# Kernel tuning notes

Hardware: AMD Instinct MI355X
Metric: run time of the kernel (lower is better)

The kernel has to match this reference:

```python
import jax, jax.numpy as jnp
import numpy as np

BS, P, D, D_WM, H, W = 64, 512, 1024, 1024, 16, 128
HD = D_WM // H
SCALE = 1.0 / np.sqrt(HD)


def setup_inputs() -> dict:
    key = jax.random.key(0)
    ks = jax.random.split(key, 10)
    s = 0.02
    x_all = jax.random.normal(ks[0], (BS, P, D), dtype=jnp.float32)
    reset_mask_all = jax.random.randint(ks[1], (BS, P), 0, 50) == 0
    return {
        'x_all': x_all,
        'reset_mask_all': reset_mask_all,
        'Wq_w': jax.random.normal(ks[2], (D, D_WM), dtype=jnp.float32) * s,
        'Wq_b': jnp.zeros((D_WM,), jnp.float32),
        'Wk_w': jax.random.normal(ks[3], (D, D_WM), dtype=jnp.float32) * s,
        'Wk_b': jnp.zeros((D_WM,), jnp.float32),
        'Wv_w': jax.random.normal(ks[4], (D, D_WM), dtype=jnp.float32) * s,
        'Wv_b': jnp.zeros((D_WM,), jnp.float32),
        'Wo_w': jax.random.normal(ks[5], (D_WM, D), dtype=jnp.float32) * s,
        'Wo_b': jnp.zeros((D,), jnp.float32),
    }


def _forward_span(x_all, reset_mask_all, Wq_w, Wq_b, Wk_w, Wk_b, Wv_w, Wv_b, Wo_w, Wo_b):
    # Batched projections over all P tokens (matches forward_span)
    q_all = jnp.einsum('bpd,de->bpe', x_all, Wq_w) + Wq_b
    k_all = jnp.einsum('bpd,de->bpe', x_all, Wk_w) + Wk_b
    v_all = jnp.einsum('bpd,de->bpe', x_all, Wv_w) + Wv_b

    def step(carry, inp):
        K, V, valid, ptr = carry  # [BS,W,D_WM], [BS,W,D_WM], [BS,W] bool, [BS] int
        q, k, v, reset_t = inp    # [BS,D_WM] x3, [BS] bool
        # doc-boundary reset
        valid = valid & ~reset_t[:, None]
        ptr = jnp.where(reset_t, 0, ptr)
        # ring-buffer write at ptr (one-hot broadcast, as in the original)
        wm = jnp.arange(W)[None, :] == ptr[:, None]          # [BS,W] bool
        wf = wm.astype(K.dtype)[:, :, None]                   # [BS,W,1]
        K = K * (1.0 - wf) + k[:, None, :] * wf
        V = V * (1.0 - wf) + v[:, None, :] * wf
        valid = valid | wm
        # windowed multi-head attention over the buffer
        qh = q.reshape(BS, H, HD)
        Kh = K.reshape(BS, W, H, HD)
        Vh = V.reshape(BS, W, H, HD)
        attn = jnp.einsum('bhd,bwhd->bhw', qh, Kh) * SCALE
        attn = jnp.where(valid[:, None, :], attn, -jnp.inf)
        attn = jax.nn.softmax(attn, axis=-1)
        attn = jnp.nan_to_num(attn)
        out = jnp.einsum('bhw,bwhd->bhd', attn, Vh).reshape(BS, D_WM)
        y = out @ Wo_w + Wo_b
        ptr = (ptr + 1) % W
        return (K, V, valid, ptr), y

    init = (
        jnp.zeros((BS, W, D_WM), x_all.dtype),
        jnp.zeros((BS, W, D_WM), x_all.dtype),
        jnp.zeros((BS, W), bool),
        jnp.zeros((BS,), jnp.int32),
    )
    xs = (
        q_all.transpose(1, 0, 2),
        k_all.transpose(1, 0, 2),
        v_all.transpose(1, 0, 2),
        reset_mask_all.T,
    )
    _, ys = jax.lax.scan(step, init, xs)  # ys: [P,BS,D]
    return ys.transpose(1, 0, 2)


def reference(x_all, reset_mask_all, Wq_w, Wq_b, Wk_w, Wk_b, Wv_w, Wv_b, Wo_w, Wo_b):
    return _forward_span(x_all, reset_mask_all, Wq_w, Wq_b, Wk_w, Wk_b, Wv_w, Wv_b, Wo_w, Wo_b)
```

## Files before the change

kernel.cpp:

```cpp
#include <hip/hip_runtime.h>
#include <stdint.h>

typedef __bf16 bf16_t;
typedef __bf16 bf16x8 __attribute__((ext_vector_type(8)));
typedef __bf16 bf16x4 __attribute__((ext_vector_type(4)));
typedef float  f32x4  __attribute__((ext_vector_type(4)));

constexpr int cBS = 64, cP = 512, cD = 1024, cDWM = 1024, cH = 16, cHD = 64, cW = 128;
constexpr int cVTP = 672;
constexpr int cM = cBS * cP;
constexpr float cSCALE = 0.125f;

__device__ __forceinline__ void gld_lds16(const void* g, void* l) {
#if __has_builtin(__builtin_amdgcn_global_load_lds)
  __builtin_amdgcn_global_load_lds(
      (__attribute__((address_space(1))) void*)g,
      (__attribute__((address_space(3))) void*)l, 16, 0, 0);
#else
  *(bf16x8*)l = *(const bf16x8*)g;
#endif
}

__global__ void cvt_x_k(const float* __restrict__ X, bf16_t* __restrict__ Y, int n) {
  int i = (blockIdx.x * blockDim.x + threadIdx.x) * 4;
  if (i >= n) return;
  float4 v = *(const float4*)(X + i);
  bf16x4 o;
  o[0] = (bf16_t)v.x; o[1] = (bf16_t)v.y; o[2] = (bf16_t)v.z; o[3] = (bf16_t)v.w;
  *(bf16x4*)(Y + i) = o;
}

__global__ void cvt_wt_k(const float* __restrict__ W0, const float* __restrict__ W1,
                         const float* __restrict__ W2, const float* __restrict__ W3,
                         bf16_t* __restrict__ T0, bf16_t* __restrict__ T1,
                         bf16_t* __restrict__ T2, bf16_t* __restrict__ T3) {
  __shared__ float tile[32][33];
  const float* Wsrc; bf16_t* Tdst;
  switch (blockIdx.z) {
    case 0: Wsrc = W0; Tdst = T0; break;
    case 1: Wsrc = W1; Tdst = T1; break;
    case 2: Wsrc = W2; Tdst = T2; break;
    default: Wsrc = W3; Tdst = T3; break;
  }
  const int n0 = blockIdx.x * 32, k0 = blockIdx.y * 32;
  const int c = threadIdx.x & 31, r8 = threadIdx.x >> 5;
#pragma unroll
  for (int q = 0; q < 4; ++q) {
    int row = r8 + q * 8;
    tile[row][c] = Wsrc[(size_t)(k0 + row) * 1024 + n0 + c];
  }
  __syncthreads();
#pragma unroll
  for (int q = 0; q < 4; ++q) {
    int row = r8 + q * 8;
    Tdst[(size_t)(n0 + row) * 1024 + k0 + c] = (bf16_t)tile[c][row];
  }
}

__global__ void resets2_k(const int* __restrict__ mask, int* __restrict__ r) {
  __shared__ int sm[cP];
  const int b = blockIdx.x, t = threadIdx.x;
  sm[t] = mask[b * cP + t] ? t : 0;
  __syncthreads();
#pragma unroll
  for (int d = 1; d < cP; d <<= 1) {
    int u = (t >= d) ? sm[t - d] : 0;
    __syncthreads();
    if (u > sm[t]) sm[t] = u;
    __syncthreads();
  }
  r[b * cP + t] = sm[t];
}

__global__ __launch_bounds__(512, 2)
void gemm_qkv8_k(const bf16_t* __restrict__ A, const bf16_t* __restrict__ Wt,
                 const float* __restrict__ bq, const float* __restrict__ bk,
                 const float* __restrict__ bvv,
                 bf16_t* __restrict__ Qh, bf16_t* __restrict__ Kh,
                 bf16_t* __restrict__ Vt) {
  __shared__ __align__(16) char LDS[131072];
  const int tid = threadIdx.x;
  const int wid = tid >> 6, ln = tid & 63;
  const int ln15 = ln & 15, g4 = ln >> 4;
  const int wr = wid >> 2, wc = wid & 3;

  const int g = blockIdx.x + 12 * blockIdx.y;
  const int xcd = g & 7, s = g >> 3;
  const int nb = s % 12, mloc = s / 12;
  const int m0 = (xcd * 16 + mloc) * 256, n0 = nb * 256;

  const bf16_t* Ab = A + (size_t)m0 * 1024;
  const bf16_t* Bb = Wt + (size_t)n0 * 1024;

  const int srow = tid >> 2;
  const int gslot = (tid & 3) ^ (srow & 3);
  const size_t aoff = (size_t)srow * 1024 + (size_t)(gslot * 8);
  char* const lbase = LDS + tid * 16;

  const int slotr = (g4 ^ (ln15 & 3)) << 4;
  const int abase = (wr * 128 + ln15) * 64 + slotr;
  const int bbase = 32768 + (wc * 64 + ln15) * 64 + slotr;

  f32x4 acc[8][4];
#pragma unroll
  for (int i = 0; i < 8; ++i)
#pragma unroll
    for (int j = 0; j < 4; ++j) acc[i][j] = {0.f, 0.f, 0.f, 0.f};

#define STAGE_A(buf, kh, j) do {                                              \
    const bf16_t* gp_ = Ab + (size_t)((j) * 64 + (kh) * 32) + aoff;           \
    char* lp_ = lbase + (buf) * 65536 + (kh) * 16384;                         \
    gld_lds16(gp_, lp_);                                                      \
    gld_lds16(gp_ + (size_t)128 * 1024, lp_ + 8192);                          \
  } while (0)

#define STAGE_B(buf, kh, j) do {                                              \
    const bf16_t* gp_ = Bb + (size_t)((j) * 64 + (kh) * 32) + aoff;           \
    char* lp_ = lbase + (buf) * 65536 + (kh) * 16384 + 32768;                 \
    gld_lds16(gp_, lp_);                                                      \
    gld_lds16(gp_ + (size_t)128 * 1024, lp_ + 8192);                          \
  } while (0)

#define NOSTAGE ((void)0)
#define VM4 asm volatile("s_waitcnt vmcnt(4)" ::: "memory")
#define VM0 asm volatile("s_waitcnt vmcnt(0)" ::: "memory")
#define NOVM ((void)0)

#define PHASE(buf, kh, qm, STAGE, VME) do {                                   \
    const char* Ar_ = LDS + (buf) * 65536 + (kh) * 16384 + abase + (qm) * 4096;\
    const char* Br_ = LDS + (buf) * 65536 + (kh) * 16384 + bbase;             \
    bf16x8 af_[4], bf_[4];                                                    \
    af_[0] = *(const bf16x8*)(Ar_);                                           \
    af_[1] = *(const bf16x8*)(Ar_ + 1024);                                    \
    af_[2] = *(const bf16x8*)(Ar_ + 2048);                                    \
    af_[3] = *(const bf16x8*)(Ar_ + 3072);                                    \
    bf_[0] = *(const bf16x8*)(Br_);                                           \
    bf_[1] = *(const bf16x8*)(Br_ + 1024);                                    \
    bf_[2] = *(const bf16x8*)(Br_ + 2048);                                    \
    bf_[3] = *(const bf16x8*)(Br_ + 3072);                                    \
    STAGE;                                                                    \
    __builtin_amdgcn_s_barrier();                                             \
    asm volatile("s_waitcnt lgkmcnt(0)" ::: "memory");                        \
    __builtin_amdgcn_s_setprio(1);                                            \
    _Pragma("unroll")                                                         \
    for (int mi4_ = 0; mi4_ < 4; ++mi4_)                                      \
      _Pragma("unroll")                                                       \
      for (int nj_ = 0; nj_ < 4; ++nj_)                                       \
        acc[(qm) * 4 + mi4_][nj_] = __builtin_amdgcn_mfma_f32_16x16x32_bf16(  \
            af_[mi4_], bf_[nj_], acc[(qm) * 4 + mi4_][nj_], 0, 0, 0);         \
    __builtin_amdgcn_s_setprio(0);                                            \
    VME;                                                                      \
    __builtin_amdgcn_s_barrier();                                             \
  } while (0)

  STAGE_A(0, 0, 0); STAGE_B(0, 0, 0); STAGE_A(0, 1, 0); STAGE_B(0, 1, 0);
  asm volatile("s_waitcnt vmcnt(4)" ::: "memory");
  __builtin_amdgcn_s_barrier();

  for (int t = 0; t < 7; ++t) {
    const int j1 = 2 * t + 1, j2 = 2 * t + 2;
    PHASE(0, 0, 0, STAGE_A(1, 0, j1), NOVM);
    PHASE(0, 0, 1, STAGE_B(1, 0, j1), VM4);
    PHASE(0, 1, 0, STAGE_A(1, 1, j1), NOVM);
    PHASE(0, 1, 1, STAGE_B(1, 1, j1), VM4);
    PHASE(1, 0, 0, STAGE_A(0, 0, j2), NOVM);
    PHASE(1, 0, 1, STAGE_B(0, 0, j2), VM4);
    PHASE(1, 1, 0, STAGE_A(0, 1, j2), NOVM);
    PHASE(1, 1, 1, STAGE_B(0, 1, j2), VM4);
  }
  PHASE(0, 0, 0, STAGE_A(1, 0, 15), NOVM);
  PHASE(0, 0, 1, STAGE_B(1, 0, 15), VM4);
  PHASE(0, 1, 0, STAGE_A(1, 1, 15), NOVM);
  PHASE(0, 1, 1, STAGE_B(1, 1, 15), VM4);
  PHASE(1, 0, 0, NOSTAGE, NOVM);
  PHASE(1, 0, 1, NOSTAGE, VM0);
  PHASE(1, 1, 0, NOSTAGE, NOVM);
  PHASE(1, 1, 1, NOSTAGE, NOVM);

#undef PHASE
#undef STAGE_A
#undef STAGE_B

  const int seg = n0 >> 10;
  const float* bias = (seg == 0) ? bq : (seg == 1) ? bk : bvv;
  bf16_t* QK = (seg == 0) ? Qh : Kh;
#pragma unroll
  for (int mi = 0; mi < 8; ++mi) {
    const int rbase = m0 + wr * 128 + mi * 16 + g4 * 4;
    const int b = rbase >> 9, pb = rbase & 511;
#pragma unroll
    for (int nj = 0; nj < 4; ++nj) {
      const int col = n0 + wc * 64 + nj * 16 + ln15;
      const int cl = col & 1023;
      const int h = cl >> 6, hd = cl & 63;
      const float bv = bias[cl];
      if (seg < 2) {
#pragma unroll
        for (int r = 0; r < 4; ++r)
          QK[(((size_t)(b * cH + h)) * cP + pb + r) * cHD + hd] =
              (bf16_t)(acc[mi][nj][r] + bv);
      } else {
        bf16x4 pk;
#pragma unroll
        for (int r = 0; r < 4; ++r) pk[r] = (bf16_t)(acc[mi][nj][r] + bv);
        *(bf16x4*)(Vt + ((size_t)((b * cH + h) * cHD + hd)) * cVTP + 128 + pb) = pk;
      }
    }
  }
}

__global__ __launch_bounds__(256)
void gemm_bt_k(const bf16_t* __restrict__ A, const bf16_t* __restrict__ Bt,
               const float* __restrict__ bias, float* __restrict__ C,
               int M, int N, int K) {
  __shared__ __align__(16) bf16_t As[2][128 * 32];
  __shared__ __align__(16) bf16_t Bs[2][128 * 32];
  const int tid = threadIdx.x;
  const int wv = tid >> 6, ln = tid & 63;
  const int ln15 = ln & 15, g4 = ln >> 4;

  const int g = blockIdx.x + 8 * blockIdx.y;
  const int xcd = g & 7, s = g >> 3;
  const int nb = s & 7, mloc = s >> 3;
  const int m0 = (xcd * 32 + mloc) * 128, n0 = nb * 128;

  const int wm = (wv >> 1) * 64, wn = (wv & 1) * 64;
  const bf16_t* Ab = A + (size_t)m0 * K;
  const bf16_t* Bb = Bt + (size_t)n0 * K;

  auto stage = [&](const bf16_t* G, bf16_t* L, int k0) {
#pragma unroll
    for (int gg = 0; gg < 2; ++gg) {
      int slot = gg * 256 + tid;
      gld_lds16(G + (size_t)(slot >> 2) * K + (k0 + (slot & 3) * 8), L + slot * 8);
    }
  };

  f32x4 acc[4][4];
#pragma unroll
  for (int i = 0; i < 4; ++i)
#pragma unroll
    for (int j = 0; j < 4; ++j) acc[i][j] = {0.f, 0.f, 0.f, 0.f};

  const int nk = K >> 5;
  stage(Ab, As[0], 0);
  stage(Bb, Bs[0], 0);
  for (int kt = 0; kt < nk; ++kt) {
    __syncthreads();
    if (kt + 1 < nk) {
      stage(Ab, As[(kt + 1) & 1], (kt + 1) * 32);
      stage(Bb, Bs[(kt + 1) & 1], (kt + 1) * 32);
    }
    const bf16_t* Asb = As[kt & 1];
    const bf16_t* Bsb = Bs[kt & 1];
    bf16x8 af[4], bfr[4];
#pragma unroll
    for (int i = 0; i < 4; ++i)
      af[i] = *(const bf16x8*)(Asb + (wm + i * 16 + ln15) * 32 + g4 * 8);
#pragma unroll
    for (int j = 0; j < 4; ++j)
      bfr[j] = *(const bf16x8*)(Bsb + (wn + j * 16 + ln15) * 32 + g4 * 8);
#pragma unroll
    for (int i = 0; i < 4; ++i)
#pragma unroll
      for (int j = 0; j < 4; ++j)
        acc[i][j] = __builtin_amdgcn_mfma_f32_16x16x32_bf16(af[i], bfr[j], acc[i][j], 0, 0, 0);
  }

#pragma unroll
  for (int i = 0; i < 4; ++i) {
    const int rbase = m0 + wm + i * 16 + g4 * 4;
#pragma unroll
    for (int j = 0; j < 4; ++j) {
      const int col = n0 + wn + j * 16 + ln15;
      const float bv = bias[col];
#pragma unroll
      for (int r = 0; r < 4; ++r)
        C[(size_t)(rbase + r) * N + col] = acc[i][j][r] + bv;
    }
  }
}

__global__ __launch_bounds__(256)
void attn3_k(const bf16_t* __restrict__ Q, const bf16_t* __restrict__ Kv,
             const bf16_t* __restrict__ Vt, const int* __restrict__ rr,
             bf16_t* __restrict__ O) {
  __shared__ __align__(16) bf16_t Pl[4][16][168];
  const int tid = threadIdx.x;
  const int wv = tid >> 6, ln = tid & 63, ln15 = ln & 15, g4 = ln >> 4;
  const int h = blockIdx.x, b = blockIdx.y, tc = blockIdx.z;
  bf16_t(*Pw)[168] = Pl[wv];
  const bf16_t* vb = Vt + ((size_t)(b * cH + h)) * cHD * cVTP;
  const bf16_t* qb = Q + ((size_t)(b * cH + h)) * cP * cHD;
  const bf16_t* kb = Kv + ((size_t)(b * cH + h)) * cP * cHD;

  for (int sub = 0; sub < 2; ++sub) {
    const int t0 = (tc * 2 + sub) * 64 + wv * 16;
    const int sbase = t0 - 128;

    int rv[4];
#pragma unroll
    for (int r = 0; r < 4; ++r) rv[r] = rr[b * cP + t0 + g4 * 4 + r];

    const bf16_t* qp = qb + (size_t)(t0 + ln15) * cHD + g4 * 8;
    const bf16x8 qa0 = *(const bf16x8*)qp;
    const bf16x8 qa1 = *(const bf16x8*)(qp + 32);

    f32x4 lg[9];
#pragma unroll
    for (int c = 0; c < 9; ++c) {
      const int s = sbase + c * 16 + ln15;
      bf16x8 k0v, k1v;
      if ((unsigned)s < (unsigned)cP) {
        const bf16_t* kp = kb + (size_t)s * cHD + g4 * 8;
        k0v = *(const bf16x8*)kp;
        k1v = *(const bf16x8*)(kp + 32);
      } else {
#pragma unroll
        for (int z = 0; z < 8; ++z) { k0v[z] = (bf16_t)0.f; k1v[z] = (bf16_t)0.f; }
      }
      f32x4 a = {0.f, 0.f, 0.f, 0.f};
      a = __builtin_amdgcn_mfma_f32_16x16x32_bf16(qa0, k0v, a, 0, 0, 0);
      a = __builtin_amdgcn_mfma_f32_16x16x32_bf16(qa1, k1v, a, 0, 0, 0);
      lg[c] = a;
    }

    float mx[4] = {-1e30f, -1e30f, -1e30f, -1e30f};
#pragma unroll
    for (int c = 0; c < 9; ++c)
#pragma unroll
      for (int r = 0; r < 4; ++r) {
        const int s = sbase + c * 16 + ln15;
        const int t = t0 + g4 * 4 + r;
        const bool ok = (s >= rv[r]) && (s <= t) && (t - s < cW);
        const float l = ok ? lg[c][r] * cSCALE : -1e30f;
        lg[c][r] = l;
        mx[r] = fmaxf(mx[r], l);
      }
#pragma unroll
    for (int r = 0; r < 4; ++r) {
      mx[r] = fmaxf(mx[r], __shfl_xor(mx[r], 1));
      mx[r] = fmaxf(mx[r], __shfl_xor(mx[r], 2));
      mx[r] = fmaxf(mx[r], __shfl_xor(mx[r], 4));
      mx[r] = fmaxf(mx[r], __shfl_xor(mx[r], 8));
    }
    float sm[4] = {0.f, 0.f, 0.f, 0.f};
#pragma unroll
    for (int c = 0; c < 9; ++c)
#pragma unroll
      for (int r = 0; r < 4; ++r) {
        const float e = __expf(lg[c][r] - mx[r]);
        lg[c][r] = e;
        sm[r] += e;
      }
#pragma unroll
    for (int r = 0; r < 4; ++r) {
      sm[r] += __shfl_xor(sm[r], 1);
      sm[r] += __shfl_xor(sm[r], 2);
      sm[r] += __shfl_xor(sm[r], 4);
      sm[r] += __shfl_xor(sm[r], 8);
    }
    float inv[4];
#pragma unroll
    for (int r = 0; r < 4; ++r) inv[r] = 1.f / sm[r];

#pragma unroll
    for (int c = 0; c < 9; ++c)
#pragma unroll
      for (int r = 0; r < 4; ++r)
        Pw[g4 * 4 + r][c * 16 + ln15] = (bf16_t)(lg[c][r] * inv[r]);
#pragma unroll
    for (int z = 0; z < 4; ++z)
      Pw[ln15][144 + g4 * 4 + z] = (bf16_t)0.f;

    f32x4 oacc[4];
#pragma unroll
    for (int j = 0; j < 4; ++j) oacc[j] = {0.f, 0.f, 0.f, 0.f};
#pragma unroll
    for (int c2 = 0; c2 < 5; ++c2) {
      const bf16x8 pa = *(const bf16x8*)(&Pw[ln15][c2 * 32 + g4 * 8]);
#pragma unroll
      for (int j = 0; j < 4; ++j) {
        const bf16x8 vf =
            *(const bf16x8*)(vb + (size_t)(j * 16 + ln15) * cVTP + (t0 + c2 * 32 + g4 * 8));
        oacc[j] = __builtin_amdgcn_mfma_f32_16x16x32_bf16(pa, vf, oacc[j], 0, 0, 0);
      }
    }
#pragma unroll
    for (int j = 0; j < 4; ++j) {
      const int col = h * cHD + j * 16 + ln15;
#pragma unroll
      for (int r = 0; r < 4; ++r)
        O[((size_t)(b * cP + t0 + g4 * 4 + r)) * cDWM + col] = (bf16_t)oacc[j][r];
    }
  }
}

extern "C" void kernel_launch(void* const* d_in, const int* in_sizes, int n_in,
                              void* d_out, int out_size, void* d_ws, size_t ws_size,
                              hipStream_t stream) {
  (void)in_sizes; (void)n_in; (void)out_size; (void)ws_size;
  const float* x  = (const float*)d_in[0];
  const int* mask = (const int*)d_in[1];
  const float* Wq = (const float*)d_in[2];
  const float* bq = (const float*)d_in[3];
  const float* Wk = (const float*)d_in[4];
  const float* bk = (const float*)d_in[5];
  const float* Wv = (const float*)d_in[6];
  const float* bv = (const float*)d_in[7];
  const float* Wo = (const float*)d_in[8];
  const float* bo = (const float*)d_in[9];
  float* out = (float*)d_out;

  char* ws = (char*)d_ws;
  size_t off = 0;
  bf16_t* Xbf = (bf16_t*)(ws + off); off += (size_t)cM * cD * 2;
  bf16_t* Wqt = (bf16_t*)(ws + off); off += (size_t)cD * cDWM * 2;
  bf16_t* Wkt = (bf16_t*)(ws + off); off += (size_t)cD * cDWM * 2;
  bf16_t* Wvt = (bf16_t*)(ws + off); off += (size_t)cD * cDWM * 2;
  bf16_t* Wot = (bf16_t*)(ws + off); off += (size_t)cDWM * cD * 2;
  bf16_t* Qh  = (bf16_t*)(ws + off); off += (size_t)cM * cDWM * 2;
  bf16_t* Kh  = (bf16_t*)(ws + off); off += (size_t)cM * cDWM * 2;
  bf16_t* Vt  = (bf16_t*)(ws + off); off += (size_t)cBS * cH * cHD * cVTP * 2;
  int* rbuf   = (int*)(ws + off);    off += (size_t)cBS * cP * 4;
  bf16_t* Ob  = Xbf;

  cvt_x_k<<<(cM * cD / 4 + 255) / 256, 256, 0, stream>>>(x, Xbf, cM * cD);
  cvt_wt_k<<<dim3(32, 32, 4), 256, 0, stream>>>(Wq, Wk, Wv, Wo, Wqt, Wkt, Wvt, Wot);
  resets2_k<<<cBS, cP, 0, stream>>>(mask, rbuf);

  gemm_qkv8_k<<<dim3(12, 128), 512, 0, stream>>>(Xbf, Wqt, bq, bk, bv, Qh, Kh, Vt);

  attn3_k<<<dim3(cH, cBS, 4), 256, 0, stream>>>(Qh, Kh, Vt, rbuf, Ob);

  gemm_bt_k<<<dim3(8, 256), 256, 0, stream>>>(Ob, Wot, bo, out, cM, cD, cDWM);
}
```

Baseline: 537.1 us.

## Use fragment-contiguous LDS layout and merge QKV GEMM phases into full-tile steps

Changes the global-to-LDS staging map so each 16-row by 32-k fragment is stored contiguously per lane, which removes the XOR swizzle and lets ds_read hit consecutive 16-byte slots. The K-loop is also restructured from eight half-tile phases per iteration to four full-tile phases: each phase loads all eight A fragments and issues 32 MFMAs, with A and B staging issued together. This halves the number of barriers and waitcnts per k-step. In exchange, register pressure rises from holding eight A fragments at once, and fewer, larger phases may overlap memory with compute less finely.

```diff
diff --git a/kernel.cpp b/kernel.cpp
--- a/kernel.cpp
+++ b/kernel.cpp
@@ -92,14 +92,14 @@
   const bf16_t* Ab = A + (size_t)m0 * 1024;
   const bf16_t* Bb = Wt + (size_t)n0 * 1024;
 
-  const int srow = tid >> 2;
-  const int gslot = (tid & 3) ^ (srow & 3);
-  const size_t aoff = (size_t)srow * 1024 + (size_t)(gslot * 8);
+  const int srow = (tid >> 6) * 16 + (tid & 15);
+  const int kc = (tid >> 4) & 3;
+  const size_t aoff = (size_t)srow * 1024 + (size_t)(kc * 8);
   char* const lbase = LDS + tid * 16;
 
-  const int slotr = (g4 ^ (ln15 & 3)) << 4;
-  const int abase = (wr * 128 + ln15) * 64 + slotr;
-  const int bbase = 32768 + (wc * 64 + ln15) * 64 + slotr;
+  const int lane16 = (g4 * 16 + ln15) * 16;
+  const int abase = (wr * 8) * 1024 + lane16;
+  const int bbase = (wc * 4) * 1024 + lane16;
 
   f32x4 acc[8][4];
 #pragma unroll
@@ -126,56 +126,47 @@
 #define VM0 asm volatile("s_waitcnt vmcnt(0)" ::: "memory")
 #define NOVM ((void)0)
 
-#define PHASE(buf, kh, qm, STAGE, VME) do {                                   \
-    const char* Ar_ = LDS + (buf) * 65536 + (kh) * 16384 + abase + (qm) * 4096;\
-    const char* Br_ = LDS + (buf) * 65536 + (kh) * 16384 + bbase;             \
-    bf16x8 af_[4], bf_[4];                                                    \
-    af_[0] = *(const bf16x8*)(Ar_);                                           \
-    af_[1] = *(const bf16x8*)(Ar_ + 1024);                                    \
-    af_[2] = *(const bf16x8*)(Ar_ + 2048);                                    \
-    af_[3] = *(const bf16x8*)(Ar_ + 3072);                                    \
-    bf_[0] = *(const bf16x8*)(Br_);                                           \
-    bf_[1] = *(const bf16x8*)(Br_ + 1024);                                    \
-    bf_[2] = *(const bf16x8*)(Br_ + 2048);                                    \
-    bf_[3] = *(const bf16x8*)(Br_ + 3072);                                    \
+#define PHASE(buf, kh, STAGE, VME) do {                                       \
+    const char* Ar_ = LDS + (buf) * 65536 + (kh) * 16384 + abase;             \
+    const char* Br_ = LDS + (buf) * 65536 + (kh) * 16384 + 32768 + bbase;     \
+    bf16x8 af_[8], bf_[4];                                                    \
+    _Pragma("unroll")                                                         \
+    for (int mi_ = 0; mi_ < 8; ++mi_)                                         \
+      af_[mi_] = *(const bf16x8*)(Ar_ + mi_ * 1024);                          \
+    _Pragma("unroll")                                                         \
+    for (int nj_ = 0; nj_ < 4; ++nj_)                                         \
+      bf_[nj_] = *(const bf16x8*)(Br_ + nj_ * 1024);                          \
     STAGE;                                                                    \
     __builtin_amdgcn_s_barrier();                                             \
     asm volatile("s_waitcnt lgkmcnt(0)" ::: "memory");                        \
     __builtin_amdgcn_s_setprio(1);                                            \
     _Pragma("unroll")                                                         \
-    for (int mi4_ = 0; mi4_ < 4; ++mi4_)                                      \
+    for (int mi_ = 0; mi_ < 8; ++mi_)                                         \
       _Pragma("unroll")                                                       \
       for (int nj_ = 0; nj_ < 4; ++nj_)                                       \
-        acc[(qm) * 4 + mi4_][nj_] = __builtin_amdgcn_mfma_f32_16x16x32_bf16(  \
-            af_[mi4_], bf_[nj_], acc[(qm) * 4 + mi4_][nj_], 0, 0, 0);         \
+        acc[mi_][nj_] = __builtin_amdgcn_mfma_f32_16x16x32_bf16(              \
+            af_[mi_], bf_[nj_], acc[mi_][nj_], 0, 0, 0);                      \
     __builtin_amdgcn_s_setprio(0);                                            \
     VME;                                                                      \
     __builtin_amdgcn_s_barrier();                                             \
   } while (0)
 
-  STAGE_A(0, 0, 0); STAGE_B(0, 0, 0); STAGE_A(0, 1, 0); STAGE_B(0, 1, 0);
-  asm volatile("s_waitcnt vmcnt(4)" ::: "memory");
+  STAGE_A(0, 0, 0); STAGE_B(0, 0, 0);
+  STAGE_A(0, 1, 0); STAGE_B(0, 1, 0);
+  VM4;
   __builtin_amdgcn_s_barrier();
 
   for (int t = 0; t < 7; ++t) {
     const int j1 = 2 * t + 1, j2 = 2 * t + 2;
-    PHASE(0, 0, 0, STAGE_A(1, 0, j1), NOVM);
-    PHASE(0, 0, 1, STAGE_B(1, 0, j1), VM4);
-    PHASE(0, 1, 0, STAGE_A(1, 1, j1), NOVM);
-    PHASE(0, 1, 1, STAGE_B(1, 1, j1), VM4);
-    PHASE(1, 0, 0, STAGE_A(0, 0, j2), NOVM);
-    PHASE(1, 0, 1, STAGE_B(0, 0, j2), VM4);
-    PHASE(1, 1, 0, STAGE_A(0, 1, j2), NOVM);
-    PHASE(1, 1, 1, STAGE_B(0, 1, j2), VM4);
-  }
-  PHASE(0, 0, 0, STAGE_A(1, 0, 15), NOVM);
-  PHASE(0, 0, 1, STAGE_B(1, 0, 15), VM4);
-  PHASE(0, 1, 0, STAGE_A(1, 1, 15), NOVM);
-  PHASE(0, 1, 1, STAGE_B(1, 1, 15), VM4);
-  PHASE(1, 0, 0, NOSTAGE, NOVM);
-  PHASE(1, 0, 1, NOSTAGE, VM0);
-  PHASE(1, 1, 0, NOSTAGE, NOVM);
-  PHASE(1, 1, 1, NOSTAGE, NOVM);
+    PHASE(0, 0, { STAGE_A(1, 0, j1); STAGE_B(1, 0, j1); }, VM4);
+    PHASE(0, 1, { STAGE_A(1, 1, j1); STAGE_B(1, 1, j1); }, VM4);
+    PHASE(1, 0, { STAGE_A(0, 0, j2); STAGE_B(0, 0, j2); }, VM4);
+    PHASE(1, 1, { STAGE_A(0, 1, j2); STAGE_B(0, 1, j2); }, VM4);
+  }
+  PHASE(0, 0, { STAGE_A(1, 0, 15); STAGE_B(1, 0, 15); }, VM4);
+  PHASE(0, 1, { STAGE_A(1, 1, 15); STAGE_B(1, 1, 15); }, VM4);
+  PHASE(1, 0, NOSTAGE, VM0);
+  PHASE(1, 1, NOSTAGE, NOVM);
 
 #undef PHASE
 #undef STAGE_A
```

Measured after the change: 544.4 us. Within noise of the previous version (+1.4%).

## Rewrite output projection GEMM with 256x256 tiles and phased 8-wave pipeline

Applied to the files above, without the earlier changes.

Replaces the 128x128, 4-wave output-projection GEMM with a 256x256 tile, 8-wave kernel that uses 128KB of LDS with XOR-swizzled layout. It splits each K-step into interleaved phases that issue async global-to-LDS loads while MFMAs run, using explicit vmcnt waits, barriers and setprio. The goal is better operand reuse, fewer LDS bank conflicts and overlap of memory with compute. In exchange, sizes are hardcoded to 1024 and the hand-scheduled waits are fragile.

```diff
diff --git a/kernel.cpp b/kernel.cpp
--- a/kernel.cpp
+++ b/kernel.cpp
@@ -209,74 +209,122 @@
   }
 }
 
-__global__ __launch_bounds__(256)
-void gemm_bt_k(const bf16_t* __restrict__ A, const bf16_t* __restrict__ Bt,
-               const float* __restrict__ bias, float* __restrict__ C,
-               int M, int N, int K) {
-  __shared__ __align__(16) bf16_t As[2][128 * 32];
-  __shared__ __align__(16) bf16_t Bs[2][128 * 32];
+__global__ __launch_bounds__(512, 2)
+void gemm_bt8_k(const bf16_t* __restrict__ A, const bf16_t* __restrict__ Bt,
+                const float* __restrict__ bias, float* __restrict__ C) {
+  __shared__ __align__(16) char LDS[131072];
   const int tid = threadIdx.x;
-  const int wv = tid >> 6, ln = tid & 63;
+  const int wid = tid >> 6, ln = tid & 63;
   const int ln15 = ln & 15, g4 = ln >> 4;
-
-  const int g = blockIdx.x + 8 * blockIdx.y;
+  const int wr = wid >> 2, wc = wid & 3;
+
+  const int g = blockIdx.x + 4 * blockIdx.y;
   const int xcd = g & 7, s = g >> 3;
-  const int nb = s & 7, mloc = s >> 3;
-  const int m0 = (xcd * 32 + mloc) * 128, n0 = nb * 128;
-
-  const int wm = (wv >> 1) * 64, wn = (wv & 1) * 64;
-  const bf16_t* Ab = A + (size_t)m0 * K;
-  const bf16_t* Bb = Bt + (size_t)n0 * K;
-
-  auto stage = [&](const bf16_t* G, bf16_t* L, int k0) {
-#pragma unroll
-    for (int gg = 0; gg < 2; ++gg) {
-      int slot = gg * 256 + tid;
-      gld_lds16(G + (size_t)(slot >> 2) * K + (k0 + (slot & 3) * 8), L + slot * 8);
-    }
-  };
-
-  f32x4 acc[4][4];
-#pragma unroll
-  for (int i = 0; i < 4; ++i)
+  const int nb = s & 3, mloc = s >> 2;
+  const int m0 = (xcd * 16 + mloc) * 256, n0 = nb * 256;
+
+  const bf16_t* Ab = A + (size_t)m0 * 1024;
+  const bf16_t* Bb = Bt + (size_t)n0 * 1024;
+
+  const int srow = tid >> 2;
+  const int gslot = (tid & 3) ^ (srow & 3);
+  const size_t aoff = (size_t)srow * 1024 + (size_t)(gslot * 8);
+  char* const lbase = LDS + tid * 16;
+
+  const int slotr = (g4 ^ (ln15 & 3)) << 4;
+  const int abase = (wr * 128 + ln15) * 64 + slotr;
+  const int bbase = 32768 + (wc * 64 + ln15) * 64 + slotr;
+
+  f32x4 acc[8][4];
+#pragma unroll
+  for (int i = 0; i < 8; ++i)
 #pragma unroll
     for (int j = 0; j < 4; ++j) acc[i][j] = {0.f, 0.f, 0.f, 0.f};
 
-  const int nk = K >> 5;
-  stage(Ab, As[0], 0);
-  stage(Bb, Bs[0], 0);
-  for (int kt = 0; kt < nk; ++kt) {
-    __syncthreads();
-    if (kt + 1 < nk) {
-      stage(Ab, As[(kt + 1) & 1], (kt + 1) * 32);
-      stage(Bb, Bs[(kt + 1) & 1], (kt + 1) * 32);
-    }
-    const bf16_t* Asb = As[kt & 1];
-    const bf16_t* Bsb = Bs[kt & 1];
-    bf16x8 af[4], bfr[4];
-#pragma unroll
-    for (int i = 0; i < 4; ++i)
-      af[i] = *(const bf16x8*)(Asb + (wm + i * 16 + ln15) * 32 + g4 * 8);
-#pragma unroll
-    for (int j = 0; j < 4; ++j)
-      bfr[j] = *(const bf16x8*)(Bsb + (wn + j * 16 + ln15) * 32 + g4 * 8);
-#pragma unroll
-    for (int i = 0; i < 4; ++i)
-#pragma unroll
-      for (int j = 0; j < 4; ++j)
-        acc[i][j] = __builtin_amdgcn_mfma_f32_16x16x32_bf16(af[i], bfr[j], acc[i][j], 0, 0, 0);
-  }
-
-#pragma unroll
-  for (int i = 0; i < 4; ++i) {
-    const int rbase = m0 + wm + i * 16 + g4 * 4;
-#pragma unroll
-    for (int j = 0; j < 4; ++j) {
-      const int col = n0 + wn + j * 16 + ln15;
+#define STAGE_A(buf, kh, j) do {                                              \
+    const bf16_t* gp_ = Ab + (size_t)((j) * 64 + (kh) * 32) + aoff;           \
+    char* lp_ = lbase + (buf) * 65536 + (kh) * 16384;                         \
+    gld_lds16(gp_, lp_);                                                      \
+    gld_lds16(gp_ + (size_t)128 * 1024, lp_ + 8192);                          \
+  } while (0)
+
+#define STAGE_B(buf, kh, j) do {                                              \
+    const bf16_t* gp_ = Bb + (size_t)((j) * 64 + (kh) * 32) + aoff;           \
+    char* lp_ = lbase + (buf) * 65536 + (kh) * 16384 + 32768;                 \
+    gld_lds16(gp_, lp_);                                                      \
+    gld_lds16(gp_ + (size_t)128 * 1024, lp_ + 8192);                          \
+  } while (0)
+
+#define NOSTAGE ((void)0)
+#define VM4 asm volatile("s_waitcnt vmcnt(4)" ::: "memory")
+#define VM0 asm volatile("s_waitcnt vmcnt(0)" ::: "memory")
+#define NOVM ((void)0)
+
+#define PHASE(buf, kh, qm, STAGE, VME) do {                                   \
+    const char* Ar_ = LDS + (buf) * 65536 + (kh) * 16384 + abase + (qm) * 4096;\
+    const char* Br_ = LDS + (buf) * 65536 + (kh) * 16384 + bbase;             \
+    bf16x8 af_[4], bf_[4];                                                    \
+    af_[0] = *(const bf16x8*)(Ar_);                                           \
+    af_[1] = *(const bf16x8*)(Ar_ + 1024);                                    \
+    af_[2] = *(const bf16x8*)(Ar_ + 2048);                                    \
+    af_[3] = *(const bf16x8*)(Ar_ + 3072);                                    \
+    bf_[0] = *(const bf16x8*)(Br_);                                           \
+    bf_[1] = *(const bf16x8*)(Br_ + 1024);                                    \
+    bf_[2] = *(const bf16x8*)(Br_ + 2048);                                    \
+    bf_[3] = *(const bf16x8*)(Br_ + 3072);                                    \
+    STAGE;                                                                    \
+    __builtin_amdgcn_s_barrier();                                             \
+    asm volatile("s_waitcnt lgkmcnt(0)" ::: "memory");                        \
+    __builtin_amdgcn_s_setprio(1);                                            \
+    _Pragma("unroll")                                                         \
+    for (int mi4_ = 0; mi4_ < 4; ++mi4_)                                      \
+      _Pragma("unroll")                                                       \
+      for (int nj_ = 0; nj_ < 4; ++nj_)                                       \
+        acc[(qm) * 4 + mi4_][nj_] = __builtin_amdgcn_mfma_f32_16x16x32_bf16(  \
+            af_[mi4_], bf_[nj_], acc[(qm) * 4 + mi4_][nj_], 0, 0, 0);         \
+    __builtin_amdgcn_s_setprio(0);                                            \
+    VME;                                                                      \
+    __builtin_amdgcn_s_barrier();                                             \
+  } while (0)
+
+  STAGE_A(0, 0, 0); STAGE_B(0, 0, 0); STAGE_A(0, 1, 0); STAGE_B(0, 1, 0);
+  asm volatile("s_waitcnt vmcnt(4)" ::: "memory");
+  __builtin_amdgcn_s_barrier();
+
+  for (int t = 0; t < 7; ++t) {
+    const int j1 = 2 * t + 1, j2 = 2 * t + 2;
+    PHASE(0, 0, 0, STAGE_A(1, 0, j1), NOVM);
+    PHASE(0, 0, 1, STAGE_B(1, 0, j1), VM4);
+    PHASE(0, 1, 0, STAGE_A(1, 1, j1), NOVM);
+    PHASE(0, 1, 1, STAGE_B(1, 1, j1), VM4);
+    PHASE(1, 0, 0, STAGE_A(0, 0, j2), NOVM);
+    PHASE(1, 0, 1, STAGE_B(0, 0, j2), VM4);
+    PHASE(1, 1, 0, STAGE_A(0, 1, j2), NOVM);
+    PHASE(1, 1, 1, STAGE_B(0, 1, j2), VM4);
+  }
+  PHASE(0, 0, 0, STAGE_A(1, 0, 15), NOVM);
+  PHASE(0, 0, 1, STAGE_B(1, 0, 15), VM4);
+  PHASE(0, 1, 0, STAGE_A(1, 1, 15), NOVM);
+  PHASE(0, 1, 1, STAGE_B(1, 1, 15), VM4);
+  PHASE(1, 0, 0, NOSTAGE, NOVM);
+  PHASE(1, 0, 1, NOSTAGE, VM0);
+  PHASE(1, 1, 0, NOSTAGE, NOVM);
+  PHASE(1, 1, 1, NOSTAGE, NOVM);
+
+#undef PHASE
+#undef STAGE_A
+#undef STAGE_B
+
+#pragma unroll
+  for (int mi = 0; mi < 8; ++mi) {
+    const int row = m0 + wr * 128 + mi * 16 + g4 * 4;
+#pragma unroll
+    for (int nj = 0; nj < 4; ++nj) {
+      const int col = n0 + wc * 64 + nj * 16 + ln15;
       const float bv = bias[col];
 #pragma unroll
       for (int r = 0; r < 4; ++r)
-        C[(size_t)(rbase + r) * N + col] = acc[i][j][r] + bv;
+        C[(size_t)(row + r) * 1024 + col] = acc[mi][nj][r] + bv;
     }
   }
 }
@@ -433,5 +481,5 @@
 
   attn3_k<<<dim3(cH, cBS, 4), 256, 0, stream>>>(Qh, Kh, Vt, rbuf, Ob);
 
-  gemm_bt_k<<<dim3(8, 256), 256, 0, stream>>>(Ob, Wot, bo, out, cM, cD, cDWM);
-}
+  gemm_bt8_k<<<dim3(4, 128), 512, 0, stream>>>(Ob, Wot, bo, out);
+}
```

New measurement: 521.3 us. 2.9% less time.
